# Performance work log

Hardware: AMD Instinct MI355X
Metric: run time of the kernel (lower is better)

## Reference

```python
import jax, jax.numpy as jnp
import numpy as np
import math

B, N, DIN, H, DH, DV, DENC, MAXLEN = 8, 1024, 1024, 8, 128, 64, 32, 1024
EPS = 1e-5


def _make_pe():
    # sinusoidal table, stored as a learnable parameter in the torch module
    pos = np.arange(MAXLEN, dtype=np.float32)[:, None]
    div = np.exp(np.arange(0, DENC, 2, dtype=np.float32) * (-math.log(10000.0) / DENC))
    pe = np.zeros((MAXLEN, DENC), np.float32)
    pe[:, 0::2] = np.sin(pos * div)
    pe[:, 1::2] = np.cos(pos * div)
    return jnp.asarray(pe)[None]  # (1, MAXLEN, DENC)


def setup_inputs() -> dict:
    key = jax.random.key(0)
    ks = jax.random.split(key, 4)
    dq = DH * H  # = d_q = d_k = 1024
    return {
        "x": jax.random.normal(ks[0], (B, N, DIN), jnp.float32),
        "gamma": jnp.ones((1, 1, DIN), jnp.float32),
        "beta": jnp.zeros((1, 1, DIN), jnp.float32),
        "pe": _make_pe(),
        "W_pos": jax.random.normal(ks[1], (DIN + DENC, DIN), jnp.float32) * 0.02,
        "b_pos": jnp.zeros((DIN,), jnp.float32),
        "W_qkv": jax.random.normal(ks[2], (DIN, 2 * dq + DV * H), jnp.float32) * 0.02,
        "b_qkv": jnp.zeros((2 * dq + DV * H,), jnp.float32),
        "W_out": jax.random.normal(ks[3], (DV * H, DIN), jnp.float32) * 0.02,
        "b_out": jnp.zeros((DIN,), jnp.float32),
        "scale": jnp.asarray(1.414, jnp.float32),
    }


def reference(x, gamma, beta, pe, W_pos, b_pos, W_qkv, b_qkv, W_out, b_out, scale):
    Bq, Nq, _ = x.shape
    # PositionalEncoding: concat sinusoidal table, project back to d_in, residual add
    pos_in = jnp.concatenate([x, jnp.broadcast_to(pe[:, :Nq], (Bq, Nq, DENC))], axis=-1)
    h = x + (pos_in @ W_pos + b_pos)
    # FeatureNorm: normalize over the SEQUENCE dim (dim=1), biased variance
    mean = h.mean(axis=1, keepdims=True)
    var = h.var(axis=1, keepdims=True)
    hn = gamma * (h - mean) * jax.lax.rsqrt(var + EPS) + beta
    # QKV projection and head split
    qkv = hn @ W_qkv + b_qkv
    dq = DH * H
    q = qkv[..., :dq].reshape(Bq, Nq, H, DH).transpose(0, 2, 1, 3)       # (B,H,N,DH)
    k = qkv[..., dq:2 * dq].reshape(Bq, Nq, H, DH).transpose(0, 2, 1, 3)  # (B,H,N,DH)
    v = qkv[..., 2 * dq:].reshape(Bq, Nq, H, DV).transpose(0, 2, 1, 3)    # (B,H,N,DV)
    # for_twdit branch: attn = softmax(-(cdist(q,k)/scale)^2) == softmax(-||q-k||^2/scale^2)
    sq = jnp.sum(q * q, axis=-1)  # (B,H,N)
    sk = jnp.sum(k * k, axis=-1)  # (B,H,N)
    d2 = sq[..., :, None] + sk[..., None, :] - 2.0 * jnp.einsum('bhnc,bhmc->bhnm', q, k)
    d2 = jnp.maximum(d2, 0.0)  # cdist is a true (nonnegative) distance
    attn = jax.nn.softmax(-d2 / (scale * scale), axis=-1)  # (B,H,N,N)
    out = jnp.einsum('bhnm,bhmd->bhnd', attn, v)            # (B,H,N,DV)
    out = out.transpose(0, 2, 1, 3).reshape(Bq, Nq, H * DV)
    return x + (out @ W_out + b_out)
```

## Files before the change

### kernel.cpp

```cpp
#include <hip/hip_runtime.h>
#include <math.h>

typedef __bf16 bf16;
typedef __attribute__((ext_vector_type(8))) __bf16 bf16x8;
typedef __attribute__((ext_vector_type(4))) float f32x4;

#define MFMA16(a, b, c) __builtin_amdgcn_mfma_f32_16x16x32_bf16(a, b, c, 0, 0, 0)

__device__ __forceinline__ void gld_lds16(const void* g, void* l) {
  __builtin_amdgcn_global_load_lds(
      (const __attribute__((address_space(1))) unsigned int*)g,
      (__attribute__((address_space(3))) unsigned int*)l, 16, 0, 0);
}

__global__ __launch_bounds__(256) void conv_bf16_kernel(const float* __restrict__ in,
                                                        bf16* __restrict__ out) {
  int idx = blockIdx.x * 256 + threadIdx.x;
  const float4 a = ((const float4*)in)[idx * 2];
  const float4 b = ((const float4*)in)[idx * 2 + 1];
  bf16x8 o = {(bf16)a.x, (bf16)a.y, (bf16)a.z, (bf16)a.w,
              (bf16)b.x, (bf16)b.y, (bf16)b.z, (bf16)b.w};
  *(bf16x8*)(out + (size_t)idx * 8) = o;
}

__global__ __launch_bounds__(256) void transpose_to_bf16(const float* __restrict__ W,
                                                         bf16* __restrict__ WT,
                                                         int K, int N) {
  __shared__ float tile[32][33];
  const int n0 = blockIdx.x * 32, k0 = blockIdx.y * 32;
  const int tx = threadIdx.x & 31, ty = threadIdx.x >> 5;
#pragma unroll
  for (int i = 0; i < 4; ++i)
    tile[ty + 8 * i][tx] = W[(size_t)(k0 + ty + 8 * i) * N + n0 + tx];
  __syncthreads();
#pragma unroll
  for (int i = 0; i < 4; ++i)
    WT[(size_t)(n0 + ty + 8 * i) * K + k0 + tx] = (bf16)tile[tx][ty + 8 * i];
}

__global__ __launch_bounds__(256) void vtrans_kernel(const bf16* __restrict__ qkv,
                                                     bf16* __restrict__ vT) {
  __shared__ bf16 tile[32][34];
  const int b = blockIdx.z;
  const int n0 = blockIdx.x * 32, c0 = blockIdx.y * 32;
  const int tx = threadIdx.x & 31, ty = threadIdx.x >> 5;
#pragma unroll
  for (int i = 0; i < 4; ++i)
    tile[ty + 8 * i][tx] = qkv[(size_t)(b * 1024 + n0 + ty + 8 * i) * 2560 + 2048 + c0 + tx];
  __syncthreads();
#pragma unroll
  for (int i = 0; i < 4; ++i)
    vT[(size_t)(b * 512 + c0 + ty + 8 * i) * 1024 + n0 + tx] = tile[tx][ty + 8 * i];
}

__global__ __launch_bounds__(256) void pe_proj_kernel(const float* __restrict__ pe,
                                                      const float* __restrict__ W_pos,
                                                      bf16* __restrict__ out) {
  int idx = blockIdx.x * 256 + threadIdx.x;
  int n = idx >> 10, c = idx & 1023;
  float s = 0.f;
#pragma unroll
  for (int e = 0; e < 32; ++e)
    s += pe[n * 32 + e] * W_pos[(size_t)(1024 + e) * 1024 + c];
  out[idx] = (bf16)s;
}

template <int NT, int OUT_BF16>
__global__ __launch_bounds__(512) void gemm_bf16(
    const bf16* __restrict__ A, const bf16* __restrict__ BT, void* __restrict__ Cout,
    int M, int N, int K,
    const float* __restrict__ bias, const float* __restrict__ add_full,
    const bf16* __restrict__ add_mod) {
  __shared__ __align__(16) bf16 As[3][128 * 64];
  __shared__ __align__(16) bf16 Bs[3][256 * 64];
  const int tid = threadIdx.x;
  const int wave = tid >> 6, lane = tid & 63;
  const int wr = wave >> 2, wc = wave & 3;
  const int lr = lane & 15, lg = lane >> 4;

  int nwg = gridDim.x * gridDim.y;
  int bid = blockIdx.y * gridDim.x + blockIdx.x;
  int s = (bid & 7) * (nwg >> 3) + (bid >> 3);
  const int row0 = (s / gridDim.x) * 128, col0 = (s % gridDim.x) * 256;

  const int trow = tid >> 3;
  const int cbd = ((tid & 7) * 16) ^ ((trow & 7) << 4);
  const bf16* asrc = A + (size_t)(row0 + trow) * K + (cbd >> 1);
  const bf16* bsrc = BT + (size_t)(col0 + trow) * K + (cbd >> 1);
  f32x4 acc[4][4] = {};

  auto STAGE = [&](int sel, int t) {
    const int kt = t * 64;
    char* al = (char*)&As[sel][0] + tid * 16;
    char* bl = (char*)&Bs[sel][0] + tid * 16;
#pragma unroll
    for (int c = 0; c < 2; ++c)
      gld_lds16(asrc + (size_t)c * 64 * K + kt, al + c * 8192);
#pragma unroll
    for (int c = 0; c < 4; ++c)
      gld_lds16(bsrc + (size_t)c * 64 * K + kt, bl + c * 8192);
  };

  STAGE(0, 0);
  if (NT > 1) STAGE(1, 1);

#pragma unroll
  for (int t = 0; t < NT; ++t) {
    if (t + 1 < NT)
      asm volatile("s_waitcnt vmcnt(6)" ::: "memory");
    else
      asm volatile("s_waitcnt vmcnt(0)" ::: "memory");
    __builtin_amdgcn_s_barrier();
    if (t + 2 < NT) STAGE((t + 2) % 3, t + 2);
    const char* Ab = (const char*)&As[t % 3][0];
    const char* Bb = (const char*)&Bs[t % 3][0];
#pragma unroll
    for (int kc = 0; kc < 2; ++kc) {
      bf16x8 af[4], bfr[4];
#pragma unroll
      for (int mt = 0; mt < 4; ++mt) {
        int r = wr * 64 + mt * 16 + lr;
        int byte = r * 128 + (((kc * 32 + lg * 8) * 2) ^ ((r & 7) << 4));
        af[mt] = *(const bf16x8*)(Ab + byte);
      }
#pragma unroll
      for (int nt = 0; nt < 4; ++nt) {
        int c = wc * 64 + nt * 16 + lr;
        int byte = c * 128 + (((kc * 32 + lg * 8) * 2) ^ ((c & 7) << 4));
        bfr[nt] = *(const bf16x8*)(Bb + byte);
      }
      __builtin_amdgcn_s_setprio(1);
#pragma unroll
      for (int mt = 0; mt < 4; ++mt)
#pragma unroll
        for (int nt = 0; nt < 4; ++nt)
          acc[mt][nt] = MFMA16(af[mt], bfr[nt], acc[mt][nt]);
      __builtin_amdgcn_s_setprio(0);
    }
  }

#pragma unroll
  for (int mt = 0; mt < 4; ++mt) {
#pragma unroll
    for (int v = 0; v < 4; ++v) {
      int r = row0 + wr * 64 + mt * 16 + lg * 4 + v;
#pragma unroll
      for (int nt = 0; nt < 4; ++nt) {
        int c = col0 + wc * 64 + nt * 16 + lr;
        float val = acc[mt][nt][v];
        if (bias) val += bias[c];
        if (add_full) val += add_full[(size_t)r * N + c];
        if (add_mod) val += (float)add_mod[(size_t)(r & 1023) * N + c];
        if (OUT_BF16)
          ((bf16*)Cout)[(size_t)r * N + c] = (bf16)val;
        else
          ((float*)Cout)[(size_t)r * N + c] = val;
      }
    }
  }
}

__global__ __launch_bounds__(512) void featnorm_kernel(const bf16* __restrict__ h,
                                                       bf16* __restrict__ hn,
                                                       const float* __restrict__ gamma,
                                                       const float* __restrict__ beta) {
  const int b = blockIdx.x >> 4;
  const int d0 = (blockIdx.x & 15) << 6;
  const int tid = threadIdx.x;
  const int c = tid & 63, g = tid >> 6;
  const size_t base = (size_t)b * (1024 * 1024) + d0 + c;
  float s = 0.f, s2 = 0.f;
  for (int n = g * 128; n < g * 128 + 128; ++n) {
    float v = (float)h[base + (size_t)n * 1024];
    s += v; s2 += v * v;
  }
  __shared__ float rs[8][64], rs2[8][64];
  rs[g][c] = s; rs2[g][c] = s2;
  __syncthreads();
  __shared__ float smean[64], srstd[64];
  if (tid < 64) {
    float S = 0.f, S2 = 0.f;
#pragma unroll
    for (int q = 0; q < 8; ++q) { S += rs[q][tid]; S2 += rs2[q][tid]; }
    float mean = S * (1.f / 1024.f);
    float var = S2 * (1.f / 1024.f) - mean * mean;
    smean[tid] = mean;
    srstd[tid] = rsqrtf(var + 1e-5f);
  }
  __syncthreads();
  const float mean = smean[c], rstd = srstd[c];
  const float gm = gamma[d0 + c], bt = beta[d0 + c];
  for (int n = g * 128; n < g * 128 + 128; ++n) {
    size_t idx = base + (size_t)n * 1024;
    hn[idx] = (bf16)(gm * ((float)h[idx] - mean) * rstd + bt);
  }
}

__global__ __launch_bounds__(256) void sk_kernel(const bf16* __restrict__ qkv,
                                                 const float* __restrict__ scale_ptr,
                                                 float* __restrict__ skl) {
  const int tid = threadIdx.x;
  const int lr = tid & 15;
  const int task = blockIdx.x * 16 + (tid >> 4);
  const int bh = task >> 10, n = task & 1023;
  const int b = bh >> 3, h = bh & 7;
  const bf16x8 v = *(const bf16x8*)(qkv + (size_t)(b * 1024 + n) * 2560 +
                                    1024 + h * 128 + lr * 8);
  float s = 0.f;
#pragma unroll
  for (int i = 0; i < 8; ++i) { float f = (float)v[i]; s += f * f; }
#pragma unroll
  for (int off = 1; off < 16; off <<= 1) s += __shfl_xor(s, off);
  if (lr == 0) {
    float sc = scale_ptr[0];
    skl[task] = s * (1.44269504f / (sc * sc));
  }
}

__global__ __launch_bounds__(256) void attn_mfma(const bf16* __restrict__ qkv,
                                                 const bf16* __restrict__ vT,
                                                 const float* __restrict__ skl,
                                                 const float* __restrict__ scale_ptr,
                                                 bf16* __restrict__ attn_o) {
  const int swz = ((blockIdx.x & 7) << 7) + (blockIdx.x >> 3);
  const int it = swz & 15, bh = swz >> 4;
  const int b = bh >> 3, h = bh & 7;
  const int i0 = it * 64;
  const int tid = threadIdx.x, wave = tid >> 6, lane = tid & 63;
  const int lr = lane & 15, lg = lane >> 4;
  const float sc = scale_ptr[0];
  const float c2 = 2.f * 1.44269504f / (sc * sc);

  __shared__ __align__(16) bf16 Ks[2][64 * 128];
  __shared__ __align__(16) bf16 Vs[2][64 * 64];
  __shared__ __align__(16) bf16 Ps[4][16 * 64];
  __shared__ float sks[1024];

  const int trowK = tid >> 4;
  const int cbKd = ((tid & 15) * 16) ^ ((trowK & 7) << 4);
  const bf16* ksrc = qkv + (size_t)(b * 1024 + trowK) * 2560 + 1024 + h * 128 + (cbKd >> 1);
  const int trowV = tid >> 3;
  const int cbVd = ((tid & 7) * 16) ^ ((trowV & 7) << 4);
  const bf16* vsrc = vT + (size_t)(b * 512 + h * 64 + trowV) * 1024 + (cbVd >> 1);

  auto STAGE = [&](int sel, int jt) {
    const bf16* kp = ksrc + (size_t)jt * 64 * 2560;
    char* kl = (char*)&Ks[sel][0] + tid * 16;
#pragma unroll
    for (int c = 0; c < 4; ++c)
      gld_lds16(kp + (size_t)c * 16 * 2560, kl + c * 4096);
    const bf16* vp = vsrc + jt * 64;
    char* vl = (char*)&Vs[sel][0] + tid * 16;
#pragma unroll
    for (int c = 0; c < 2; ++c)
      gld_lds16(vp + c * 32 * 1024, vl + c * 4096);
  };

  {
    float4 sv = ((const float4*)(skl + (size_t)bh * 1024))[tid];
    *(float4*)&sks[tid * 4] = sv;
  }
  bf16x8 qf[4];
  {
    const bf16* qrow = qkv + (size_t)(b * 1024 + i0 + wave * 16 + lr) * 2560 + h * 128;
#pragma unroll
    for (int kc = 0; kc < 4; ++kc) qf[kc] = *(const bf16x8*)(qrow + kc * 32 + lg * 8);
  }
  __syncthreads();

  bf16x8 vones;
  {
    bf16 one_or_zero = (lr == 0) ? (bf16)1.0f : (bf16)0.0f;
#pragma unroll
    for (int i = 0; i < 8; ++i) vones[i] = one_or_zero;
  }

  f32x4 o[4] = {};
  f32x4 o_l = {};

  STAGE(0, 0);
  asm volatile("s_waitcnt vmcnt(0)" ::: "memory");
  __builtin_amdgcn_s_barrier();

#pragma unroll
  for (int jt = 0; jt < 16; ++jt) {
    const int cur = jt & 1;
    if (jt < 15) STAGE(cur ^ 1, jt + 1);

    f32x4 sacc[4] = {};
    __builtin_amdgcn_s_setprio(1);
#pragma unroll
    for (int kc = 0; kc < 4; ++kc) {
#pragma unroll
      for (int nt = 0; nt < 4; ++nt) {
        int j = nt * 16 + lr;
        int byte = j * 256 + (((kc * 32 + lg * 8) * 2) ^ ((j & 7) << 4));
        bf16x8 kf = *(const bf16x8*)((const char*)&Ks[cur][0] + byte);
        sacc[nt] = MFMA16(qf[kc], kf, sacc[nt]);
      }
    }
    __builtin_amdgcn_s_setprio(0);

#pragma unroll
    for (int nt = 0; nt < 4; ++nt) {
      float skv = sks[jt * 64 + nt * 16 + lr];
#pragma unroll
      for (int v = 0; v < 4; ++v) {
        float p = __builtin_amdgcn_exp2f(sacc[nt][v] * c2 - skv);
        int r = lg * 4 + v, c = nt * 16 + lr;
        int byte = r * 128 + ((c * 2) ^ ((r & 7) << 4));
        *(bf16*)((char*)&Ps[wave][0] + byte) = (bf16)p;
      }
    }
    bf16x8 pf[2];
#pragma unroll
    for (int kc = 0; kc < 2; ++kc) {
      int byte = lr * 128 + (((kc * 32 + lg * 8) * 2) ^ ((lr & 7) << 4));
      pf[kc] = *(const bf16x8*)((const char*)&Ps[wave][0] + byte);
    }
    __builtin_amdgcn_s_setprio(1);
#pragma unroll
    for (int kc = 0; kc < 2; ++kc) {
#pragma unroll
      for (int nt = 0; nt < 4; ++nt) {
        int d = nt * 16 + lr;
        int byte = d * 128 + (((kc * 32 + lg * 8) * 2) ^ ((d & 7) << 4));
        bf16x8 vf = *(const bf16x8*)((const char*)&Vs[cur][0] + byte);
        o[nt] = MFMA16(pf[kc], vf, o[nt]);
      }
      o_l = MFMA16(pf[kc], vones, o_l);
    }
    __builtin_amdgcn_s_setprio(0);

    asm volatile("s_waitcnt vmcnt(0)" ::: "memory");
    __builtin_amdgcn_s_barrier();
  }

#pragma unroll
  for (int v = 0; v < 4; ++v) {
    float ls = __shfl(o_l[v], lg << 4);
    float inv = 1.f / ls;
    int r = i0 + wave * 16 + lg * 4 + v;
#pragma unroll
    for (int nt = 0; nt < 4; ++nt) {
      int c = h * 64 + nt * 16 + lr;
      attn_o[(size_t)(b * 1024 + r) * 512 + c] = (bf16)(o[nt][v] * inv);
    }
  }
}

extern "C" void kernel_launch(void* const* d_in, const int* in_sizes, int n_in,
                              void* d_out, int out_size, void* d_ws, size_t ws_size,
                              hipStream_t stream) {
  const float* x     = (const float*)d_in[0];
  const float* gamma = (const float*)d_in[1];
  const float* beta  = (const float*)d_in[2];
  const float* pe    = (const float*)d_in[3];
  const float* W_pos = (const float*)d_in[4];
  const float* b_pos = (const float*)d_in[5];
  const float* W_qkv = (const float*)d_in[6];
  const float* b_qkv = (const float*)d_in[7];
  const float* W_out = (const float*)d_in[8];
  const float* b_out = (const float*)d_in[9];
  const float* scale = (const float*)d_in[10];
  float* outp = (float*)d_out;

  char* ws = (char*)d_ws;
  const size_t MB = 1 << 20;
  bf16* x_bf   = (bf16*)(ws);
  bf16* hn     = (bf16*)(ws);
  bf16* wpos_t = (bf16*)(ws + 16 * MB);
  bf16* wqkv_t = (bf16*)(ws + 18 * MB);
  bf16* wout_t = (bf16*)(ws + 23 * MB);
  bf16* pe_pj  = (bf16*)(ws + 24 * MB);
  bf16* vT     = (bf16*)(ws + 24 * MB);
  bf16* h      = (bf16*)(ws + 32 * MB);
  bf16* attn_o = (bf16*)(ws + 32 * MB);
  bf16* qkv    = (bf16*)(ws + 48 * MB);
  float* skl   = (float*)(ws + 88 * MB);

  conv_bf16_kernel<<<4096, 256, 0, stream>>>(x, x_bf);
  transpose_to_bf16<<<dim3(32, 32), 256, 0, stream>>>(W_pos, wpos_t, 1024, 1024);
  transpose_to_bf16<<<dim3(80, 32), 256, 0, stream>>>(W_qkv, wqkv_t, 1024, 2560);
  transpose_to_bf16<<<dim3(32, 16), 256, 0, stream>>>(W_out, wout_t, 512, 1024);
  pe_proj_kernel<<<4096, 256, 0, stream>>>(pe, W_pos, pe_pj);
  gemm_bf16<16, 1><<<dim3(4, 64), 512, 0, stream>>>(x_bf, wpos_t, h, 8192, 1024, 1024,
                                                    b_pos, x, pe_pj);
  featnorm_kernel<<<128, 512, 0, stream>>>(h, hn, gamma, beta);
  gemm_bf16<16, 1><<<dim3(10, 64), 512, 0, stream>>>(hn, wqkv_t, qkv, 8192, 2560, 1024,
                                                     b_qkv, nullptr, nullptr);
  sk_kernel<<<4096, 256, 0, stream>>>(qkv, scale, skl);
  vtrans_kernel<<<dim3(32, 16, 8), 256, 0, stream>>>(qkv, vT);
  attn_mfma<<<1024, 256, 0, stream>>>(qkv, vT, skl, scale, attn_o);
  gemm_bf16<8, 0><<<dim3(4, 64), 512, 0, stream>>>(attn_o, wout_t, outp, 8192, 1024, 512,
                                                   b_out, x, nullptr);
}
```

Measured before the change: 275.0 us.

## Reshape GEMM tile to 256x128 with split-phase staging and runtime K loop

The block GEMM tile changes from 128x256 to 256x128, with the warp grid now 4x2 instead of 2x4. Each K step is split into two half-phases, so half of the next-next stage's loads are issued between two MFMA groups with a barrier in between. The loop count is now a runtime value (K>>6) rather than a template parameter, so the main loop is no longer fully unrolled. The aim is to interleave global-to-LDS traffic with MFMA work more finely. The cost is an extra barrier per iteration and possible loss of unroll-driven scheduling.

```diff
diff --git a/kernel.cpp b/kernel.cpp
--- a/kernel.cpp
+++ b/kernel.cpp
@@ -65,23 +65,23 @@
   out[idx] = (bf16)s;
 }
 
-template <int NT, int OUT_BF16>
-__global__ __launch_bounds__(512) void gemm_bf16(
+template <int OUT_BF16>
+__global__ __launch_bounds__(512) void gemm8(
     const bf16* __restrict__ A, const bf16* __restrict__ BT, void* __restrict__ Cout,
     int M, int N, int K,
     const float* __restrict__ bias, const float* __restrict__ add_full,
     const bf16* __restrict__ add_mod) {
-  __shared__ __align__(16) bf16 As[3][128 * 64];
-  __shared__ __align__(16) bf16 Bs[3][256 * 64];
+  __shared__ __align__(16) bf16 As[3][256 * 64];
+  __shared__ __align__(16) bf16 Bs[3][128 * 64];
   const int tid = threadIdx.x;
   const int wave = tid >> 6, lane = tid & 63;
-  const int wr = wave >> 2, wc = wave & 3;
+  const int wr = wave >> 1, wc = wave & 1;
   const int lr = lane & 15, lg = lane >> 4;
 
   int nwg = gridDim.x * gridDim.y;
   int bid = blockIdx.y * gridDim.x + blockIdx.x;
   int s = (bid & 7) * (nwg >> 3) + (bid >> 3);
-  const int row0 = (s / gridDim.x) * 128, col0 = (s % gridDim.x) * 256;
+  const int row0 = (s / gridDim.x) * 256, col0 = (s % gridDim.x) * 128;
 
   const int trow = tid >> 3;
   const int cbd = ((tid & 7) * 16) ^ ((trow & 7) << 4);
@@ -89,72 +89,100 @@
   const bf16* bsrc = BT + (size_t)(col0 + trow) * K + (cbd >> 1);
   f32x4 acc[4][4] = {};
 
-  auto STAGE = [&](int sel, int t) {
+  const int NT = K >> 6;
+
+  auto STAGEH = [&](int r, int t, int half) {
     const int kt = t * 64;
-    char* al = (char*)&As[sel][0] + tid * 16;
-    char* bl = (char*)&Bs[sel][0] + tid * 16;
-#pragma unroll
-    for (int c = 0; c < 2; ++c)
+    char* al = (char*)&As[r][0] + tid * 16;
+    char* bl = (char*)&Bs[r][0] + tid * 16;
+#pragma unroll
+    for (int c = 2 * half; c < 2 * half + 2; ++c)
       gld_lds16(asrc + (size_t)c * 64 * K + kt, al + c * 8192);
-#pragma unroll
-    for (int c = 0; c < 4; ++c)
-      gld_lds16(bsrc + (size_t)c * 64 * K + kt, bl + c * 8192);
+    gld_lds16(bsrc + (size_t)half * 64 * K + kt, bl + half * 8192);
   };
 
-  STAGE(0, 0);
-  if (NT > 1) STAGE(1, 1);
-
-#pragma unroll
-  for (int t = 0; t < NT; ++t) {
-    if (t + 1 < NT)
+  STAGEH(0, 0, 0); STAGEH(0, 0, 1);
+  STAGEH(1, 1, 0); STAGEH(1, 1, 1);
+  asm volatile("s_waitcnt vmcnt(6)" ::: "memory");
+  __builtin_amdgcn_s_barrier();
+
+  for (int T = 0; T < NT; ++T) {
+    const int r = T % 3;
+    const char* Ab = (const char*)&As[r][0];
+    const char* Bb = (const char*)&Bs[r][0];
+
+    if (T + 2 < NT) STAGEH((T + 2) % 3, T + 2, 0);
+    bf16x8 bfr[4][2], af0[2][2];
+#pragma unroll
+    for (int nt = 0; nt < 4; ++nt)
+#pragma unroll
+      for (int ks = 0; ks < 2; ++ks) {
+        int row = wc * 64 + nt * 16 + lr;
+        bfr[nt][ks] = *(const bf16x8*)(Bb + row * 128 +
+                                       (((ks * 32 + lg * 8) * 2) ^ ((row & 7) << 4)));
+      }
+#pragma unroll
+    for (int mt = 0; mt < 2; ++mt)
+#pragma unroll
+      for (int ks = 0; ks < 2; ++ks) {
+        int row = wr * 64 + mt * 16 + lr;
+        af0[mt][ks] = *(const bf16x8*)(Ab + row * 128 +
+                                       (((ks * 32 + lg * 8) * 2) ^ ((row & 7) << 4)));
+      }
+    __builtin_amdgcn_s_setprio(1);
+#pragma unroll
+    for (int mt = 0; mt < 2; ++mt)
+#pragma unroll
+      for (int nt = 0; nt < 4; ++nt)
+#pragma unroll
+        for (int ks = 0; ks < 2; ++ks)
+          acc[mt][nt] = MFMA16(af0[mt][ks], bfr[nt][ks], acc[mt][nt]);
+    __builtin_amdgcn_s_setprio(0);
+    __builtin_amdgcn_s_barrier();
+
+    if (T + 2 < NT) STAGEH((T + 2) % 3, T + 2, 1);
+    bf16x8 af1[2][2];
+#pragma unroll
+    for (int mt = 0; mt < 2; ++mt)
+#pragma unroll
+      for (int ks = 0; ks < 2; ++ks) {
+        int row = wr * 64 + (2 + mt) * 16 + lr;
+        af1[mt][ks] = *(const bf16x8*)(Ab + row * 128 +
+                                       (((ks * 32 + lg * 8) * 2) ^ ((row & 7) << 4)));
+      }
+    __builtin_amdgcn_s_setprio(1);
+#pragma unroll
+    for (int mt = 0; mt < 2; ++mt)
+#pragma unroll
+      for (int nt = 0; nt < 4; ++nt)
+#pragma unroll
+        for (int ks = 0; ks < 2; ++ks)
+          acc[2 + mt][nt] = MFMA16(af1[mt][ks], bfr[nt][ks], acc[2 + mt][nt]);
+    __builtin_amdgcn_s_setprio(0);
+
+    if (T < NT - 2)
       asm volatile("s_waitcnt vmcnt(6)" ::: "memory");
-    else
+    else if (T == NT - 2)
       asm volatile("s_waitcnt vmcnt(0)" ::: "memory");
     __builtin_amdgcn_s_barrier();
-    if (t + 2 < NT) STAGE((t + 2) % 3, t + 2);
-    const char* Ab = (const char*)&As[t % 3][0];
-    const char* Bb = (const char*)&Bs[t % 3][0];
-#pragma unroll
-    for (int kc = 0; kc < 2; ++kc) {
-      bf16x8 af[4], bfr[4];
-#pragma unroll
-      for (int mt = 0; mt < 4; ++mt) {
-        int r = wr * 64 + mt * 16 + lr;
-        int byte = r * 128 + (((kc * 32 + lg * 8) * 2) ^ ((r & 7) << 4));
-        af[mt] = *(const bf16x8*)(Ab + byte);
-      }
-#pragma unroll
-      for (int nt = 0; nt < 4; ++nt) {
-        int c = wc * 64 + nt * 16 + lr;
-        int byte = c * 128 + (((kc * 32 + lg * 8) * 2) ^ ((c & 7) << 4));
-        bfr[nt] = *(const bf16x8*)(Bb + byte);
-      }
-      __builtin_amdgcn_s_setprio(1);
-#pragma unroll
-      for (int mt = 0; mt < 4; ++mt)
-#pragma unroll
-        for (int nt = 0; nt < 4; ++nt)
-          acc[mt][nt] = MFMA16(af[mt], bfr[nt], acc[mt][nt]);
-      __builtin_amdgcn_s_setprio(0);
-    }
   }
 
 #pragma unroll
   for (int mt = 0; mt < 4; ++mt) {
 #pragma unroll
     for (int v = 0; v < 4; ++v) {
-      int r = row0 + wr * 64 + mt * 16 + lg * 4 + v;
+      int r2 = row0 + wr * 64 + mt * 16 + lg * 4 + v;
 #pragma unroll
       for (int nt = 0; nt < 4; ++nt) {
         int c = col0 + wc * 64 + nt * 16 + lr;
         float val = acc[mt][nt][v];
         if (bias) val += bias[c];
-        if (add_full) val += add_full[(size_t)r * N + c];
-        if (add_mod) val += (float)add_mod[(size_t)(r & 1023) * N + c];
+        if (add_full) val += add_full[(size_t)r2 * N + c];
+        if (add_mod) val += (float)add_mod[(size_t)(r2 & 1023) * N + c];
         if (OUT_BF16)
-          ((bf16*)Cout)[(size_t)r * N + c] = (bf16)val;
+          ((bf16*)Cout)[(size_t)r2 * N + c] = (bf16)val;
         else
-          ((float*)Cout)[(size_t)r * N + c] = val;
+          ((float*)Cout)[(size_t)r2 * N + c] = val;
       }
     }
   }
@@ -384,14 +412,14 @@
   transpose_to_bf16<<<dim3(80, 32), 256, 0, stream>>>(W_qkv, wqkv_t, 1024, 2560);
   transpose_to_bf16<<<dim3(32, 16), 256, 0, stream>>>(W_out, wout_t, 512, 1024);
   pe_proj_kernel<<<4096, 256, 0, stream>>>(pe, W_pos, pe_pj);
-  gemm_bf16<16, 1><<<dim3(4, 64), 512, 0, stream>>>(x_bf, wpos_t, h, 8192, 1024, 1024,
-                                                    b_pos, x, pe_pj);
+  gemm8<1><<<dim3(8, 32), 512, 0, stream>>>(x_bf, wpos_t, h, 8192, 1024, 1024,
+                                            b_pos, x, pe_pj);
   featnorm_kernel<<<128, 512, 0, stream>>>(h, hn, gamma, beta);
-  gemm_bf16<16, 1><<<dim3(10, 64), 512, 0, stream>>>(hn, wqkv_t, qkv, 8192, 2560, 1024,
-                                                     b_qkv, nullptr, nullptr);
+  gemm8<1><<<dim3(20, 32), 512, 0, stream>>>(hn, wqkv_t, qkv, 8192, 2560, 1024,
+                                             b_qkv, nullptr, nullptr);
   sk_kernel<<<4096, 256, 0, stream>>>(qkv, scale, skl);
   vtrans_kernel<<<dim3(32, 16, 8), 256, 0, stream>>>(qkv, vT);
   attn_mfma<<<1024, 256, 0, stream>>>(qkv, vT, skl, scale, attn_o);
-  gemm_bf16<8, 0><<<dim3(4, 64), 512, 0, stream>>>(attn_o, wout_t, outp, 8192, 1024, 512,
-                                                   b_out, x, nullptr);
-}
+  gemm8<0><<<dim3(8, 32), 512, 0, stream>>>(attn_o, wout_t, outp, 8192, 1024, 512,
+                                            b_out, x, nullptr);
+}
```

Measured after the change: 321.4 us. 1.17x slower.

## Restructure GEMM to 4 waves with K=32 tiles, k-major LDS layout, 2 blocks/CU

Applied to the files above, without the earlier changes.

The bf16 GEMM now uses 256 threads (4 waves) instead of 512. Each wave computes a 128x64 sub-tile with 8x4 MFMA accumulators, and the K step drops to 32 with a triple-buffered LDS stored k-chunk-major rather than XOR-swizzled. Halving LDS per block and setting launch bounds to 2 blocks per CU aims to raise occupancy and cut barrier count per MFMA. The cost is twice as many accumulator registers per wave and a new LDS layout that may cause bank conflicts or register pressure.

```diff
diff --git a/kernel.cpp b/kernel.cpp
--- a/kernel.cpp
+++ b/kernel.cpp
@@ -66,84 +66,80 @@
 }
 
 template <int NT, int OUT_BF16>
-__global__ __launch_bounds__(512) void gemm_bf16(
+__global__ __launch_bounds__(256, 2) void gemm_p(
     const bf16* __restrict__ A, const bf16* __restrict__ BT, void* __restrict__ Cout,
     int M, int N, int K,
     const float* __restrict__ bias, const float* __restrict__ add_full,
     const bf16* __restrict__ add_mod) {
-  __shared__ __align__(16) bf16 As[3][128 * 64];
-  __shared__ __align__(16) bf16 Bs[3][256 * 64];
+  __shared__ __align__(16) bf16 As[3][128 * 32];
+  __shared__ __align__(16) bf16 Bs[3][256 * 32];
   const int tid = threadIdx.x;
-  const int wave = tid >> 6, lane = tid & 63;
-  const int wr = wave >> 2, wc = wave & 3;
+  const int wc = tid >> 6, lane = tid & 63;
   const int lr = lane & 15, lg = lane >> 4;
 
-  int nwg = gridDim.x * gridDim.y;
-  int bid = blockIdx.y * gridDim.x + blockIdx.x;
-  int s = (bid & 7) * (nwg >> 3) + (bid >> 3);
+  const int nwg = gridDim.x * gridDim.y;
+  const int bid = blockIdx.y * gridDim.x + blockIdx.x;
+  const int s = (bid & 7) * (nwg >> 3) + (bid >> 3);
   const int row0 = (s / gridDim.x) * 128, col0 = (s % gridDim.x) * 256;
 
-  const int trow = tid >> 3;
-  const int cbd = ((tid & 7) * 16) ^ ((trow & 7) << 4);
-  const bf16* asrc = A + (size_t)(row0 + trow) * K + (cbd >> 1);
-  const bf16* bsrc = BT + (size_t)(col0 + trow) * K + (cbd >> 1);
-  f32x4 acc[4][4] = {};
+  const bf16* asrc = A + (size_t)(row0 + (tid & 127)) * K + (tid >> 7) * 8;
+  const bf16* bsrc = BT + (size_t)(col0 + tid) * K;
+  f32x4 acc[8][4] = {};
 
   auto STAGE = [&](int sel, int t) {
-    const int kt = t * 64;
+    const int kt = t * 32;
     char* al = (char*)&As[sel][0] + tid * 16;
     char* bl = (char*)&Bs[sel][0] + tid * 16;
-#pragma unroll
-    for (int c = 0; c < 2; ++c)
-      gld_lds16(asrc + (size_t)c * 64 * K + kt, al + c * 8192);
+    gld_lds16(asrc + kt, al);
+    gld_lds16(asrc + kt + 16, al + 4096);
 #pragma unroll
     for (int c = 0; c < 4; ++c)
-      gld_lds16(bsrc + (size_t)c * 64 * K + kt, bl + c * 8192);
+      gld_lds16(bsrc + kt + c * 8, bl + c * 4096);
   };
 
   STAGE(0, 0);
-  if (NT > 1) STAGE(1, 1);
-
-#pragma unroll
-  for (int t = 0; t < NT; ++t) {
-    if (t + 1 < NT)
+  STAGE(1, 1);
+  asm volatile("s_waitcnt vmcnt(6)" ::: "memory");
+  __builtin_amdgcn_s_barrier();
+
+  int cur = 0;
+  for (int T = 0; T < NT; ++T) {
+    if (T + 2 < NT) {
+      int s2 = cur + 2; if (s2 >= 3) s2 -= 3;
+      STAGE(s2, T + 2);
+    }
+    const char* Ab = (const char*)As + cur * (128 * 32 * 2);
+    const char* Bb = (const char*)Bs + cur * (256 * 32 * 2);
+
+    bf16x8 bfr[4], af[8];
+#pragma unroll
+    for (int nt = 0; nt < 4; ++nt)
+      bfr[nt] = *(const bf16x8*)(Bb + lg * 4096 + (wc * 64 + nt * 16 + lr) * 16);
+#pragma unroll
+    for (int mt = 0; mt < 8; ++mt)
+      af[mt] = *(const bf16x8*)(Ab + lg * 2048 + (mt * 16 + lr) * 16);
+
+    __builtin_amdgcn_s_setprio(1);
+#pragma unroll
+    for (int mt = 0; mt < 8; ++mt)
+#pragma unroll
+      for (int nt = 0; nt < 4; ++nt)
+        acc[mt][nt] = MFMA16(af[mt], bfr[nt], acc[mt][nt]);
+    __builtin_amdgcn_s_setprio(0);
+
+    if (T + 2 < NT)
       asm volatile("s_waitcnt vmcnt(6)" ::: "memory");
     else
       asm volatile("s_waitcnt vmcnt(0)" ::: "memory");
     __builtin_amdgcn_s_barrier();
-    if (t + 2 < NT) STAGE((t + 2) % 3, t + 2);
-    const char* Ab = (const char*)&As[t % 3][0];
-    const char* Bb = (const char*)&Bs[t % 3][0];
-#pragma unroll
-    for (int kc = 0; kc < 2; ++kc) {
-      bf16x8 af[4], bfr[4];
-#pragma unroll
-      for (int mt = 0; mt < 4; ++mt) {
-        int r = wr * 64 + mt * 16 + lr;
-        int byte = r * 128 + (((kc * 32 + lg * 8) * 2) ^ ((r & 7) << 4));
-        af[mt] = *(const bf16x8*)(Ab + byte);
-      }
-#pragma unroll
-      for (int nt = 0; nt < 4; ++nt) {
-        int c = wc * 64 + nt * 16 + lr;
-        int byte = c * 128 + (((kc * 32 + lg * 8) * 2) ^ ((c & 7) << 4));
-        bfr[nt] = *(const bf16x8*)(Bb + byte);
-      }
-      __builtin_amdgcn_s_setprio(1);
-#pragma unroll
-      for (int mt = 0; mt < 4; ++mt)
-#pragma unroll
-        for (int nt = 0; nt < 4; ++nt)
-          acc[mt][nt] = MFMA16(af[mt], bfr[nt], acc[mt][nt]);
-      __builtin_amdgcn_s_setprio(0);
-    }
-  }
-
-#pragma unroll
-  for (int mt = 0; mt < 4; ++mt) {
+    cur = (cur == 2) ? 0 : cur + 1;
+  }
+
+#pragma unroll
+  for (int mt = 0; mt < 8; ++mt) {
 #pragma unroll
     for (int v = 0; v < 4; ++v) {
-      int r = row0 + wr * 64 + mt * 16 + lg * 4 + v;
+      int r = row0 + mt * 16 + lg * 4 + v;
 #pragma unroll
       for (int nt = 0; nt < 4; ++nt) {
         int c = col0 + wc * 64 + nt * 16 + lr;
@@ -384,14 +380,14 @@
   transpose_to_bf16<<<dim3(80, 32), 256, 0, stream>>>(W_qkv, wqkv_t, 1024, 2560);
   transpose_to_bf16<<<dim3(32, 16), 256, 0, stream>>>(W_out, wout_t, 512, 1024);
   pe_proj_kernel<<<4096, 256, 0, stream>>>(pe, W_pos, pe_pj);
-  gemm_bf16<16, 1><<<dim3(4, 64), 512, 0, stream>>>(x_bf, wpos_t, h, 8192, 1024, 1024,
-                                                    b_pos, x, pe_pj);
+  gemm_p<32, 1><<<dim3(4, 64), 256, 0, stream>>>(x_bf, wpos_t, h, 8192, 1024, 1024,
+                                                 b_pos, x, pe_pj);
   featnorm_kernel<<<128, 512, 0, stream>>>(h, hn, gamma, beta);
-  gemm_bf16<16, 1><<<dim3(10, 64), 512, 0, stream>>>(hn, wqkv_t, qkv, 8192, 2560, 1024,
-                                                     b_qkv, nullptr, nullptr);
+  gemm_p<32, 1><<<dim3(10, 64), 256, 0, stream>>>(hn, wqkv_t, qkv, 8192, 2560, 1024,
+                                                  b_qkv, nullptr, nullptr);
   sk_kernel<<<4096, 256, 0, stream>>>(qkv, scale, skl);
   vtrans_kernel<<<dim3(32, 16, 8), 256, 0, stream>>>(qkv, vT);
   attn_mfma<<<1024, 256, 0, stream>>>(qkv, vT, skl, scale, attn_o);
-  gemm_bf16<8, 0><<<dim3(4, 64), 512, 0, stream>>>(attn_o, wout_t, outp, 8192, 1024, 512,
-                                                   b_out, x, nullptr);
-}
+  gemm_p<16, 0><<<dim3(4, 64), 256, 0, stream>>>(attn_o, wout_t, outp, 8192, 1024, 512,
+                                                 b_out, x, nullptr);
+}
```

Result: slower. 411.2 us (+49.5%).
